# Kernel optimization log

Measured on AMD Instinct MI355X. Metric: run time of the kernel, lower is better.

## Reference

```python
import jax, jax.numpy as jnp
import numpy as np

B, T, D = 4, 8192, 1024
C = 8.0


def setup_inputs() -> dict:
    key = jax.random.key(0)
    k1, k2, k3 = jax.random.split(key, 3)
    init_std = D ** (-0.5)
    x = jax.random.normal(k1, (B, T, D), dtype=jnp.float32)
    W_in = jax.random.truncated_normal(k2, -3.0, 3.0, (D, D), dtype=jnp.float32) * init_std
    W_gate = jax.random.truncated_normal(k3, -3.0, 3.0, (D, D), dtype=jnp.float32) * init_std
    b_in = jnp.zeros((D,), dtype=jnp.float32)
    b_gate = jnp.zeros((D,), dtype=jnp.float32)
    forget_lambda = jnp.linspace(-4.323, -9.0, D, dtype=jnp.float32)
    return {"x": x, "W_in": W_in, "b_in": b_in, "W_gate": W_gate,
            "b_gate": b_gate, "forget_lambda": forget_lambda}


def _combine(c1, c2):
    # linear recurrence h_t = a_t * h_{t-1} + b_t  (associative composition)
    a1, b1 = c1
    a2, b2 = c2
    return a1 * a2, a2 * b1 + b2


def reference(x, W_in, b_in, W_gate, b_gate, forget_lambda):
    # x: [B, T, D]
    input_gate = x @ W_in.T + b_in          # [B, T, D]
    recurrence_gate = x @ W_gate.T + b_gate  # [B, T, D]
    alpha = jnp.exp(-C * jax.nn.softplus(forget_lambda) * jax.nn.sigmoid(recurrence_gate))
    beta = jnp.sqrt(1.0 - alpha ** 2 + 1e-6)
    xbeta = beta * jax.nn.sigmoid(input_gate) * x
    # parallel scan of h_t = alpha_t * h_{t-1} + xbeta_t along sequence axis
    _, h = jax.lax.associative_scan(_combine, (alpha, xbeta), axis=1)
    return h
```

## Files before the change

### kernel.cpp

```cpp
#include <hip/hip_runtime.h>

typedef unsigned short u16;
typedef __attribute__((ext_vector_type(8))) short short8;
typedef __attribute__((ext_vector_type(4))) float f32x4;

#define T_SEQ 8192
#define DDIM 1024
#define BB 4
#define MM (BB * T_SEQ)
#define NC 128
#define CHUNK (T_SEQ / NC)
#define CHAINS (BB * DDIM)
#define NT 16
#define NHT 32

__device__ __forceinline__ float bf_lo(unsigned p) {
    union { unsigned u; float f; } v; v.u = p << 16; return v.f;
}
__device__ __forceinline__ float bf_hi(unsigned p) {
    union { unsigned u; float f; } v; v.u = p & 0xffff0000u; return v.f;
}
__device__ __forceinline__ float bf_u16(u16 p) {
    union { unsigned u; float f; } v; v.u = ((unsigned)p) << 16; return v.f;
}
__device__ __forceinline__ u16 f2bf(float f) {
    union { unsigned u; float f; } v; v.f = f;
    unsigned r = v.u + 0x7fffu + ((v.u >> 16) & 1u);
    return (u16)(r >> 16);
}
__device__ __forceinline__ float sigm(float z) {
    return __builtin_amdgcn_rcpf(1.0f + __expf(-z));
}
__device__ __forceinline__ void gld16(const u16* g, u16* l) {
    __builtin_amdgcn_global_load_lds((const __attribute__((address_space(1))) void*)g,
                                     (__attribute__((address_space(3))) void*)l, 16, 0, 0);
}

#define N4X (MM * DDIM / 4)
#define N4W (DDIM * DDIM / 4)
__global__ __launch_bounds__(256) void cvt_all(const float* __restrict__ x,
                                               const float* __restrict__ Wi,
                                               const float* __restrict__ Wg,
                                               u16* __restrict__ Xb,
                                               u16* __restrict__ Wib,
                                               u16* __restrict__ Wgb) {
    int i = blockIdx.x * 256 + threadIdx.x;
    const float* src; u16* dst; int j;
    if (i < N4X)            { src = x;  dst = Xb;  j = i; }
    else if (i < N4X + N4W) { src = Wi; dst = Wib; j = i - N4X; }
    else                    { src = Wg; dst = Wgb; j = i - N4X - N4W; }
    float4 v = ((const float4*)src)[j];
    ushort4 o;
    o.x = f2bf(v.x); o.y = f2bf(v.y); o.z = f2bf(v.z); o.w = f2bf(v.w);
    ((ushort4*)dst)[j] = o;
}


#define MROW(i_, av)                                                                   \
    acc[i_][0] = __builtin_amdgcn_mfma_f32_16x16x32_bf16(av, b0, acc[i_][0], 0, 0, 0); \
    acc[i_][1] = __builtin_amdgcn_mfma_f32_16x16x32_bf16(av, b1, acc[i_][1], 0, 0, 0); \
    acc[i_][2] = __builtin_amdgcn_mfma_f32_16x16x32_bf16(av, b2, acc[i_][2], 0, 0, 0); \
    acc[i_][3] = __builtin_amdgcn_mfma_f32_16x16x32_bf16(av, b3, acc[i_][3], 0, 0, 0);

#define MALL MROW(0, a0) MROW(1, a1) MROW(2, a2) MROW(3, a3) \
             MROW(4, a4) MROW(5, a5) MROW(6, a6) MROW(7, a7)

#define LDA_H(h_, i) (*(const short8*)&lds[((h_)&3)*8192 + (arow0 + (i)*16)*32 + aoff])
#define LDB_H(h_, j) (*(const short8*)&lds[32768 + ((h_)&3)*8192 + (brow0 + (j)*16)*32 + aoff])

#define RD_H(h_)                                                                       \
    b0 = LDB_H(h_, 0); b1 = LDB_H(h_, 1); b2 = LDB_H(h_, 2); b3 = LDB_H(h_, 3);        \
    a0 = LDA_H(h_, 0); a1 = LDA_H(h_, 1); a2 = LDA_H(h_, 2); a3 = LDA_H(h_, 3);        \
    a4 = LDA_H(h_, 4); a5 = LDA_H(h_, 5); a6 = LDA_H(h_, 6); a7 = LDA_H(h_, 7);

#define STA_H(h_, rb) gld16(gA + (size_t)(h_)*32 + (size_t)(rb)*128*DDIM,              \
                            &lds[((h_)&3)*8192 + (rb)*4096 + tid*8])
#define STB_H(h_, hf) gld16(((hf) ? gBg : gBi) + (size_t)(h_)*32,                      \
                            &lds[32768 + ((h_)&3)*8192 + (hf)*4096 + tid*8])
#define ST_H(h_) STA_H(h_, 0); STA_H(h_, 1); STB_H(h_, 0); STB_H(h_, 1);

__global__ __launch_bounds__(512, 2)
void gemm_fused(const u16* __restrict__ X, const u16* __restrict__ Wi,
                const u16* __restrict__ Wg, const float* __restrict__ b_in,
                const float* __restrict__ b_gate, const float* __restrict__ lam,
                u16* __restrict__ Sg, u16* __restrict__ XBg) {
    const int bid = blockIdx.x;
    const int xcd = bid & 7;
    const int r = bid >> 3;
    const int n_tile = r & 7;
    const int m_tile = xcd * 16 + (r >> 3);
    const int tN0 = n_tile * 128;
    const int tM0 = m_tile * 256;

    const int tid = threadIdx.x;
    const int lane = tid & 63;
    const int w = tid >> 6;
    const int wm = w >> 2;
    const int wn = w & 3;
    const int gate = wn >> 1;
    const int wn_sub = wn & 1;

    __shared__ u16 lds[65536];

    const int srow = tid >> 2;
    const int c8log = (tid & 3) ^ ((tid >> 3) & 3);
    const u16* gA  = X  + (size_t)(tM0 + srow) * DDIM + c8log * 8;
    const u16* gBi = Wi + (size_t)(tN0 + srow) * DDIM + c8log * 8;
    const u16* gBg = Wg + (size_t)(tN0 + srow) * DDIM + c8log * 8;

    const int lm = lane & 15;
    const int aoff = (((lane >> 4) ^ ((lm >> 1) & 3))) * 8;
    const int arow0 = wm * 128 + lm;
    const int brow0 = gate * 128 + wn_sub * 64 + lm;

    f32x4 acc[8][4] = {};
    short8 a0, a1, a2, a3, a4, a5, a6, a7, b0, b1, b2, b3;

    ST_H(0) ST_H(1) ST_H(2)

    for (int h = 0; h < NHT - 3; ++h) {
        asm volatile("s_waitcnt vmcnt(8)" ::: "memory");
        __builtin_amdgcn_s_barrier();
        RD_H(h)
        ST_H(h + 3)
        __builtin_amdgcn_s_setprio(1);
        MALL
        __builtin_amdgcn_s_setprio(0);
    }
    {
        asm volatile("s_waitcnt vmcnt(8)" ::: "memory");
        __builtin_amdgcn_s_barrier();
        RD_H(29)
        __builtin_amdgcn_s_setprio(1);
        MALL
        __builtin_amdgcn_s_setprio(0);
    }
    {
        asm volatile("s_waitcnt vmcnt(4)" ::: "memory");
        __builtin_amdgcn_s_barrier();
        RD_H(30)
        __builtin_amdgcn_s_setprio(1);
        MALL
        __builtin_amdgcn_s_setprio(0);
    }
    {
        asm volatile("s_waitcnt vmcnt(0)" ::: "memory");
        __builtin_amdgcn_s_barrier();
        RD_H(31)
        __builtin_amdgcn_s_setprio(1);
        MALL
        __builtin_amdgcn_s_setprio(0);
    }
    __builtin_amdgcn_s_barrier();

    const int r0 = (lane >> 4) << 2;
    const int cb = lane & 15;
    if (gate) {
#pragma unroll
        for (int j = 0; j < 4; ++j) {
            const int colg = tN0 + wn_sub * 64 + j * 16 + cb;
            const int cl = wn_sub * 64 + j * 16 + cb;
            const float bj = b_gate[colg];
            const float nsp = -8.0f * log1pf(__expf(lam[colg]));
#pragma unroll
            for (int i = 0; i < 8; ++i) {
                const int rl0 = wm * 128 + i * 16 + r0;
#pragma unroll
                for (int rr = 0; rr < 4; ++rr) {
                    const int rl = rl0 + rr;
                    float s = nsp * sigm(acc[i][j][rr] + bj);
                    lds[rl * 128 + (cl ^ (((rl >> 2) & 7) << 4))] = f2bf(s);
                }
            }
        }
    } else {
#pragma unroll
        for (int j = 0; j < 4; ++j) {
            const int colg = tN0 + wn_sub * 64 + j * 16 + cb;
            const int cl = wn_sub * 64 + j * 16 + cb;
            const float bj = b_in[colg];
#pragma unroll
            for (int i = 0; i < 8; ++i) {
                const int rl0 = wm * 128 + i * 16 + r0;
#pragma unroll
                for (int rr = 0; rr < 4; ++rr) {
                    const int rl = rl0 + rr;
                    float p = sigm(acc[i][j][rr] + bj);
                    lds[32768 + rl * 128 + (cl ^ (((rl >> 2) & 7) << 4))] =
                        (u16)(p * 65535.0f + 0.5f);
                }
            }
        }
    }
    asm volatile("s_waitcnt lgkmcnt(0)" ::: "memory");
    __builtin_amdgcn_s_barrier();
    __builtin_amdgcn_sched_barrier(0);

    const int cc = tid & 15;
    const int rg0 = (tid >> 4) * 8;
#pragma unroll
    for (int k = 0; k < 8; ++k) {
        const int rl = rg0 + k;
        const int ch = (cc ^ (((rl >> 2) & 7) << 1)) * 8;
        short8 sv = *(const short8*)&lds[rl * 128 + ch];
        short8 pv = *(const short8*)&lds[32768 + rl * 128 + ch];
        const size_t go = (size_t)(tM0 + rl) * DDIM + tN0 + cc * 8;
        short8 xv = *(const short8*)&X[go];
        short8 ov;
#pragma unroll
        for (int e = 0; e < 8; ++e) {
            float s = bf_u16((u16)sv[e]);
            float p = (float)((u16)pv[e]) * (1.0f / 65535.0f);
            float xf = bf_u16((u16)xv[e]);
            float be = sqrtf(1.0f - __expf(2.0f * s) + 1e-6f);
            ov[e] = (short)f2bf(be * p * xf);
        }
        *(short8*)&Sg[go] = sv;
        *(short8*)&XBg[go] = ov;
    }
}

__global__ __launch_bounds__(256)
void scan_pass1(const u16* __restrict__ S, const u16* __restrict__ XB,
                float* __restrict__ AggA, float* __restrict__ AggB) {
    const int c = blockIdx.x, dblk = blockIdx.y, bq = blockIdx.z;
    const int d0 = dblk * 512 + threadIdx.x * 2;
    size_t base = ((size_t)(bq * T_SEQ + c * CHUNK)) * DDIM + d0;

    float A0 = 1.0f, B0 = 0.0f, A1 = 1.0f, B1 = 0.0f;
#pragma unroll 8
    for (int t = 0; t < CHUNK; t++) {
        unsigned sp = *(const unsigned*)(S + base);
        unsigned xp = *(const unsigned*)(XB + base);
        float a0 = __expf(bf_lo(sp));
        float a1 = __expf(bf_hi(sp));
        B0 = fmaf(a0, B0, bf_lo(xp)); A0 *= a0;
        B1 = fmaf(a1, B1, bf_hi(xp)); A1 *= a1;
        base += DDIM;
    }
    const int chain = bq * DDIM + d0;
    float2 av; av.x = A0; av.y = A1;
    float2 bv; bv.x = B0; bv.y = B1;
    *(float2*)(AggA + (size_t)c * CHAINS + chain) = av;
    *(float2*)(AggB + (size_t)c * CHAINS + chain) = bv;
}

__global__ __launch_bounds__(256)
void scan_pass2(const float* __restrict__ AggA, const float* __restrict__ AggB,
                float* __restrict__ H0) {
    const int chain = blockIdx.x * 256 + threadIdx.x;
    float p = 0.0f;
#pragma unroll 8
    for (int c = 0; c < NC; c++) {
        H0[(size_t)c * CHAINS + chain] = p;
        p = AggA[(size_t)c * CHAINS + chain] * p + AggB[(size_t)c * CHAINS + chain];
    }
}

__global__ __launch_bounds__(256)
void scan_pass3(const u16* __restrict__ S, const u16* __restrict__ XB,
                const float* __restrict__ H0, float* __restrict__ out) {
    const int c = blockIdx.x, dblk = blockIdx.y, bq = blockIdx.z;
    const int d0 = dblk * 512 + threadIdx.x * 2;
    size_t base = ((size_t)(bq * T_SEQ + c * CHUNK)) * DDIM + d0;
    const int chain = bq * DDIM + d0;

    float2 h = *(const float2*)(H0 + (size_t)c * CHAINS + chain);
#pragma unroll 8
    for (int t = 0; t < CHUNK; t++) {
        unsigned sp = *(const unsigned*)(S + base);
        unsigned xp = *(const unsigned*)(XB + base);
        float a0 = __expf(bf_lo(sp));
        float a1 = __expf(bf_hi(sp));
        h.x = fmaf(a0, h.x, bf_lo(xp));
        h.y = fmaf(a1, h.y, bf_hi(xp));
        *(float2*)(out + base) = h;
        base += DDIM;
    }
}

extern "C" void kernel_launch(void* const* d_in, const int* in_sizes, int n_in,
                              void* d_out, int out_size, void* d_ws, size_t ws_size,
                              hipStream_t stream) {
    const float* x   = (const float*)d_in[0];
    const float* Win = (const float*)d_in[1];
    const float* bin = (const float*)d_in[2];
    const float* Wg  = (const float*)d_in[3];
    const float* bg  = (const float*)d_in[4];
    const float* lam = (const float*)d_in[5];
    float* out = (float*)d_out;

    char* w = (char*)d_ws;
    u16* Wi_bf  = (u16*)(w);
    u16* Wg_bf  = (u16*)(w + (size_t)(2) * 1024 * 1024);
    u16* Sg     = (u16*)(w + (size_t)(4) * 1024 * 1024);
    u16* XBg    = (u16*)(w + (size_t)(68) * 1024 * 1024);
    float* AggA = (float*)(w + (size_t)(132) * 1024 * 1024);
    float* AggB = (float*)(w + (size_t)(134) * 1024 * 1024);
    float* H0   = (float*)(w + (size_t)(136) * 1024 * 1024);

    u16* Xbf = (u16*)d_out;

    cvt_all<<<dim3((N4X + 2 * N4W) / 256), dim3(256), 0, stream>>>(
        x, Win, Wg, Xbf, Wi_bf, Wg_bf);

    gemm_fused<<<dim3((DDIM / 128) * (MM / 256)), dim3(512), 0, stream>>>(
        Xbf, Wi_bf, Wg_bf, bin, bg, lam, Sg, XBg);

    scan_pass1<<<dim3(NC, 2, BB), dim3(256), 0, stream>>>(Sg, XBg, AggA, AggB);
    scan_pass2<<<dim3(CHAINS / 256), dim3(256), 0, stream>>>(AggA, AggB, H0);
    scan_pass3<<<dim3(NC, 2, BB), dim3(256), 0, stream>>>(Sg, XBg, H0, out);
}
```

Measured before the change: 474.4 us.

## Split GEMM k-step into two barrier-separated phases with interleaved loads

Restructures the GEMM main loop so each k-slice runs in two halves: the first half reads B and four A fragments from LDS, issues the A global-to-LDS prefetch, and runs four MFMA rows; the second half reads the remaining A fragments, issues the B prefetch, and runs the other four rows. Explicit stage indices and barriers with lgkmcnt waits and sched_barrier replace the modulo-indexed loop, in a ping-pong style that lets waves overlap LDS reads, global loads and MFMA work. This lowers register pressure (fewer live fragments) but adds four barriers per k-step instead of one.

New measurement: 467.0 us. No clear change (-1.6%).

```diff
diff --git a/kernel.cpp b/kernel.cpp
--- a/kernel.cpp
+++ b/kernel.cpp
@@ -11,7 +11,6 @@
 #define NC 128
 #define CHUNK (T_SEQ / NC)
 #define CHAINS (BB * DDIM)
-#define NT 16
 #define NHT 32
 
 __device__ __forceinline__ float bf_lo(unsigned p) {
@@ -62,22 +61,41 @@
     acc[i_][2] = __builtin_amdgcn_mfma_f32_16x16x32_bf16(av, b2, acc[i_][2], 0, 0, 0); \
     acc[i_][3] = __builtin_amdgcn_mfma_f32_16x16x32_bf16(av, b3, acc[i_][3], 0, 0, 0);
 
-#define MALL MROW(0, a0) MROW(1, a1) MROW(2, a2) MROW(3, a3) \
-             MROW(4, a4) MROW(5, a5) MROW(6, a6) MROW(7, a7)
-
-#define LDA_H(h_, i) (*(const short8*)&lds[((h_)&3)*8192 + (arow0 + (i)*16)*32 + aoff])
-#define LDB_H(h_, j) (*(const short8*)&lds[32768 + ((h_)&3)*8192 + (brow0 + (j)*16)*32 + aoff])
-
-#define RD_H(h_)                                                                       \
-    b0 = LDB_H(h_, 0); b1 = LDB_H(h_, 1); b2 = LDB_H(h_, 2); b3 = LDB_H(h_, 3);        \
-    a0 = LDA_H(h_, 0); a1 = LDA_H(h_, 1); a2 = LDA_H(h_, 2); a3 = LDA_H(h_, 3);        \
-    a4 = LDA_H(h_, 4); a5 = LDA_H(h_, 5); a6 = LDA_H(h_, 6); a7 = LDA_H(h_, 7);
-
-#define STA_H(h_, rb) gld16(gA + (size_t)(h_)*32 + (size_t)(rb)*128*DDIM,              \
-                            &lds[((h_)&3)*8192 + (rb)*4096 + tid*8])
-#define STB_H(h_, hf) gld16(((hf) ? gBg : gBi) + (size_t)(h_)*32,                      \
-                            &lds[32768 + ((h_)&3)*8192 + (hf)*4096 + tid*8])
-#define ST_H(h_) STA_H(h_, 0); STA_H(h_, 1); STB_H(h_, 0); STB_H(h_, 1);
+#define LDA_S(s_, i) (*(const short8*)&lds[(s_)*8192 + (arow0 + (i)*16)*32 + aoff])
+#define LDB_S(s_, j) (*(const short8*)&lds[32768 + (s_)*8192 + (brow0 + (j)*16)*32 + aoff])
+
+#define STA_S(ds_, ht_, rb) gld16(gA + (size_t)(ht_)*32 + (size_t)(rb)*128*DDIM,       \
+                                  &lds[(ds_)*8192 + (rb)*4096 + tid*8])
+#define STB_S(ds_, ht_, hf) gld16(((hf) ? gBg : gBi) + (size_t)(ht_)*32,               \
+                                  &lds[32768 + (ds_)*8192 + (hf)*4096 + tid*8])
+
+#define PHASE_A(s_, ds_, ht_, DOST)                                                    \
+    b0 = LDB_S(s_, 0); b1 = LDB_S(s_, 1); b2 = LDB_S(s_, 2); b3 = LDB_S(s_, 3);        \
+    a0 = LDA_S(s_, 0); a1 = LDA_S(s_, 1); a2 = LDA_S(s_, 2); a3 = LDA_S(s_, 3);        \
+    if (DOST) { STA_S(ds_, ht_, 0); STA_S(ds_, ht_, 1); }                              \
+    __builtin_amdgcn_s_barrier();                                                      \
+    asm volatile("s_waitcnt lgkmcnt(0)" ::: "memory");                                 \
+    __builtin_amdgcn_sched_barrier(0);                                                 \
+    __builtin_amdgcn_s_setprio(1);                                                     \
+    MROW(0, a0) MROW(1, a1) MROW(2, a2) MROW(3, a3)                                    \
+    __builtin_amdgcn_s_setprio(0);                                                     \
+    __builtin_amdgcn_s_barrier();
+
+#define PHASE_B(s_, ds_, ht_, DOST, VMS)                                               \
+    a0 = LDA_S(s_, 4); a1 = LDA_S(s_, 5); a2 = LDA_S(s_, 6); a3 = LDA_S(s_, 7);        \
+    if (DOST) { STB_S(ds_, ht_, 0); STB_S(ds_, ht_, 1); }                              \
+    asm volatile("s_waitcnt " VMS ::: "memory");                                       \
+    __builtin_amdgcn_s_barrier();                                                      \
+    asm volatile("s_waitcnt lgkmcnt(0)" ::: "memory");                                 \
+    __builtin_amdgcn_sched_barrier(0);                                                 \
+    __builtin_amdgcn_s_setprio(1);                                                     \
+    MROW(4, a0) MROW(5, a1) MROW(6, a2) MROW(7, a3)                                    \
+    __builtin_amdgcn_s_setprio(0);                                                     \
+    __builtin_amdgcn_s_barrier();
+
+#define PAIR(s_, ds_, ht_, DOST, VMS)                                                  \
+    PHASE_A(s_, ds_, ht_, DOST)                                                        \
+    PHASE_B(s_, ds_, ht_, DOST, VMS)
 
 __global__ __launch_bounds__(512, 2)
 void gemm_fused(const u16* __restrict__ X, const u16* __restrict__ Wi,
@@ -114,44 +132,25 @@
     const int brow0 = gate * 128 + wn_sub * 64 + lm;
 
     f32x4 acc[8][4] = {};
-    short8 a0, a1, a2, a3, a4, a5, a6, a7, b0, b1, b2, b3;
-
-    ST_H(0) ST_H(1) ST_H(2)
-
-    for (int h = 0; h < NHT - 3; ++h) {
-        asm volatile("s_waitcnt vmcnt(8)" ::: "memory");
-        __builtin_amdgcn_s_barrier();
-        RD_H(h)
-        ST_H(h + 3)
-        __builtin_amdgcn_s_setprio(1);
-        MALL
-        __builtin_amdgcn_s_setprio(0);
-    }
-    {
-        asm volatile("s_waitcnt vmcnt(8)" ::: "memory");
-        __builtin_amdgcn_s_barrier();
-        RD_H(29)
-        __builtin_amdgcn_s_setprio(1);
-        MALL
-        __builtin_amdgcn_s_setprio(0);
-    }
-    {
-        asm volatile("s_waitcnt vmcnt(4)" ::: "memory");
-        __builtin_amdgcn_s_barrier();
-        RD_H(30)
-        __builtin_amdgcn_s_setprio(1);
-        MALL
-        __builtin_amdgcn_s_setprio(0);
-    }
-    {
-        asm volatile("s_waitcnt vmcnt(0)" ::: "memory");
-        __builtin_amdgcn_s_barrier();
-        RD_H(31)
-        __builtin_amdgcn_s_setprio(1);
-        MALL
-        __builtin_amdgcn_s_setprio(0);
-    }
+    short8 a0, a1, a2, a3, b0, b1, b2, b3;
+
+    STA_S(0, 0, 0); STA_S(0, 0, 1); STB_S(0, 0, 0); STB_S(0, 0, 1);
+    STA_S(1, 1, 0); STA_S(1, 1, 1); STB_S(1, 1, 0); STB_S(1, 1, 1);
+    STA_S(2, 2, 0); STA_S(2, 2, 1); STB_S(2, 2, 0); STB_S(2, 2, 1);
+    asm volatile("s_waitcnt vmcnt(8)" ::: "memory");
     __builtin_amdgcn_s_barrier();
+
+    for (int g = 0; g < 7; ++g) {
+        const int hb = 4 * g;
+        PAIR(0, 3, hb + 3, 1, "vmcnt(8)")
+        PAIR(1, 0, hb + 4, 1, "vmcnt(8)")
+        PAIR(2, 1, hb + 5, 1, "vmcnt(8)")
+        PAIR(3, 2, hb + 6, 1, "vmcnt(8)")
+    }
+    PAIR(0, 3, 31, 1, "vmcnt(8)")
+    PAIR(1, 0, 0, 0, "vmcnt(4)")
+    PAIR(2, 0, 0, 0, "vmcnt(0)")
+    PAIR(3, 0, 0, 0, "vmcnt(0)")
 
     const int r0 = (lane >> 4) << 2;
     const int cb = lane & 15;
```
